# Kernel optimization log

Measured on AMD Instinct MI355X. Metric: run time of the kernel, lower is better.

The kernel has to match this reference:

```python
import jax, jax.numpy as jnp
import numpy as np

B, S, E, H, D = 2, 4096, 512, 8, 64  # batch, seq, embed, heads, key_dim


def setup_inputs() -> dict:
    key = jax.random.key(0)
    ks = jax.random.split(key, 8)
    queries = jax.random.normal(ks[0], (B, S, E), dtype=jnp.float32)
    keys = jax.random.normal(ks[1], (B, S, E), dtype=jnp.float32)
    values = jax.random.normal(ks[2], (B, S, E), dtype=jnp.float32)
    mask = jax.random.randint(ks[3], (B, H, S, S), 0, 2).astype(bool)
    scale = 1.0 / np.sqrt(E)
    Wq = jax.random.normal(ks[4], (E, H * D), dtype=jnp.float32) * scale
    Wk = jax.random.normal(ks[5], (E, H * D), dtype=jnp.float32) * scale
    Wv = jax.random.normal(ks[6], (E, H * D), dtype=jnp.float32) * scale
    Wo = jax.random.normal(ks[7], (H * D, E), dtype=jnp.float32) * scale
    return {"queries": queries, "keys": keys, "values": values, "mask": mask,
            "Wq": Wq, "Wk": Wk, "Wv": Wv, "Wo": Wo}


def reference(queries, keys, values, mask, Wq, Wk, Wv, Wo):
    # QKV projections (no bias), reshape to heads: (B, S, H, D)
    q = (queries @ Wq).reshape(B, -1, H, D)
    k = (keys @ Wk).reshape(B, -1, H, D)
    v = (values @ Wv).reshape(B, -1, H, D)
    # scores: (B, H, Sq, Sk)
    scores = jnp.einsum("bqhd,bkhd->bhqk", q, k) / jnp.sqrt(jnp.float32(D))
    scores = jnp.where(mask, jnp.float32(-1e10), scores)
    attn = jax.nn.softmax(scores, axis=-1)
    out = jnp.einsum("bhqk,bkhd->bqhd", attn, v).reshape(B, -1, H * D)
    return out @ Wo
```

## Files before the change

### kernel.cpp

```cpp
#include <hip/hip_runtime.h>
#include <hip/hip_bf16.h>

#define NB 2
#define NS 4096
#define NE 512
#define NH 8
#define ND 64
#define NHD 512

typedef __attribute__((ext_vector_type(8))) short short8;
typedef __attribute__((ext_vector_type(4))) float floatx4;

#define MFMA16(a, b, c) __builtin_amdgcn_mfma_f32_16x16x32_bf16((a), (b), (c), 0, 0, 0)

union Cvt8 { uint4 u; short8 s; };
static __device__ __forceinline__ short8 ld8(const __hip_bfloat16* p) {
  Cvt8 c; c.u = *(const uint4*)p; return c.s;
}
union BH { __hip_bfloat16 h; short s; };
static __device__ __forceinline__ short f2bs(float x) {
  BH u; u.h = __float2bfloat16(x); return u.s;
}

__global__ __launch_bounds__(256) void mask_pack(const int* __restrict__ mask,
                                                 unsigned long long* __restrict__ bits) {
  const int lane = threadIdx.x & 63;
  const long wid = (long)((blockIdx.x * 256 + threadIdx.x) >> 6);
  const long base = wid * 512;
  const int* p = mask + base * 64 + lane;
  for (int i = 0; i < 512; i += 4) {
    const int m0 = p[(long)(i + 0) * 64];
    const int m1 = p[(long)(i + 1) * 64];
    const int m2 = p[(long)(i + 2) * 64];
    const int m3 = p[(long)(i + 3) * 64];
    const unsigned long long b0 = __ballot(m0 != 0);
    const unsigned long long b1 = __ballot(m1 != 0);
    const unsigned long long b2 = __ballot(m2 != 0);
    const unsigned long long b3 = __ballot(m3 != 0);
    if (lane == 0) {
      *(ulonglong2*)(bits + base + i) = ulonglong2{b0, b1};
      *(ulonglong2*)(bits + base + i + 2) = ulonglong2{b2, b3};
    }
  }
}

__global__ __launch_bounds__(256) void wconv(
    const float* w0, const float* w1, const float* w2, const float* w3,
    __hip_bfloat16* t0, __hip_bfloat16* t1,
    __hip_bfloat16* t2, __hip_bfloat16* t3) {
  __shared__ __hip_bfloat16 tile[64][72];
  const float* src;
  __hip_bfloat16* dst;
  switch (blockIdx.z) {
    case 0: src = w0; dst = t0; break;
    case 1: src = w1; dst = t1; break;
    case 2: src = w2; dst = t2; break;
    default: src = w3; dst = t3; break;
  }
  const int tx = threadIdx.x & 63, ty = threadIdx.x >> 6;
  const int n0 = blockIdx.x * 64, k0 = blockIdx.y * 64;
  for (int r = ty; r < 64; r += 4)
    tile[r][tx] = __float2bfloat16(src[(long)(k0 + r) * 512 + n0 + tx]);
  __syncthreads();
  for (int r = ty; r < 64; r += 4)
    dst[(long)(n0 + r) * 512 + k0 + tx] = tile[tx][r];
}

__global__ __launch_bounds__(256) void gemm_qkv(
    const float* A0, const float* A1, const float* A2,
    const __hip_bfloat16* W0, const __hip_bfloat16* W1, const __hip_bfloat16* W2,
    __hip_bfloat16* O0, __hip_bfloat16* O1, __hip_bfloat16* O2) {
  const float* A;
  const __hip_bfloat16* Wt;
  __hip_bfloat16* O;
  switch (blockIdx.z) {
    case 0: A = A0; Wt = W0; O = O0; break;
    case 1: A = A1; Wt = W1; O = O1; break;
    default: A = A2; Wt = W2; O = O2; break;
  }
  const int lane = threadIdx.x & 63;
  const int w = threadIdx.x >> 6;
  const int c = lane & 15, g = lane >> 4;
  const int m0 = blockIdx.x * 64 + w * 16;
  const int n0 = blockIdx.y * 64;

  floatx4 acc[4] = {};
  const float* ap = A + (long)(m0 + c) * 512 + g * 8;
  const __hip_bfloat16* wp = Wt + (long)(n0 + c) * 512 + g * 8;
  for (int ks = 0; ks < 512; ks += 32) {
    const float4 f0 = *(const float4*)(ap + ks);
    const float4 f1 = *(const float4*)(ap + ks + 4);
    short8 a;
    a[0] = f2bs(f0.x); a[1] = f2bs(f0.y); a[2] = f2bs(f0.z); a[3] = f2bs(f0.w);
    a[4] = f2bs(f1.x); a[5] = f2bs(f1.y); a[6] = f2bs(f1.z); a[7] = f2bs(f1.w);
#pragma unroll
    for (int t = 0; t < 4; ++t) {
      short8 b = ld8(wp + t * 16 * 512 + ks);
      acc[t] = MFMA16(a, b, acc[t]);
    }
  }
  const float sc = (blockIdx.z == 0) ? 0.125f : 1.0f;
#pragma unroll
  for (int t = 0; t < 4; ++t) {
#pragma unroll
    for (int r = 0; r < 4; ++r) {
      const int m = m0 + g * 4 + r;
      const int n = n0 + t * 16 + c;
      const int bb = m >> 12, s = m & 4095, h = n >> 6, d = n & 63;
      O[(((long)bb * NH + h) * NS + s) * ND + d] = __float2bfloat16(acc[t][r] * sc);
    }
  }
}

#define VPAD 72
__device__ __forceinline__ int vswz(int row) { return ((row >> 3) & 7) * 8; }

__global__ __launch_bounds__(256) void flash_attn(
    const __hip_bfloat16* Q, const __hip_bfloat16* K, const __hip_bfloat16* V,
    const unsigned long long* __restrict__ Mb, __hip_bfloat16* AO) {
  __shared__ __hip_bfloat16 Ks[64 * VPAD];
  __shared__ __hip_bfloat16 Vt[64 * VPAD];
  __shared__ __hip_bfloat16 Pb[4 * 16 * VPAD];

  const int tid = threadIdx.x;
  const int lane = tid & 63, w = tid >> 6;
  const int c = lane & 15, g = lane >> 4;
  const int bz = blockIdx.z, hy = blockIdx.y;
  const int q0 = blockIdx.x * 64 + w * 16;
  const long headbase = ((long)bz * NH + hy) * NS;
  const unsigned long long* mrp0 = Mb + ((headbase + q0 + g * 4) << 6);

  const short8 qf0 = ld8(Q + (headbase + q0 + c) * ND + g * 8);
  const short8 qf1 = ld8(Q + (headbase + q0 + c) * ND + 32 + g * 8);

  floatx4 oacc[4] = {};
  float m_i[4], l_i[4];
#pragma unroll
  for (int r = 0; r < 4; ++r) { m_i[r] = -1e30f; l_i[r] = 0.f; }
  __hip_bfloat16* Pw = Pb + w * 16 * VPAD;

  for (int kt = 0; kt < 64; ++kt) {
    const int k0 = kt * 64;
#pragma unroll
    for (int it = 0; it < 2; ++it) {
      const int chunk = tid + it * 256;
      const int kc = chunk >> 3;
      const int dd = (chunk & 7) * 8;
      const long gbase = (headbase + k0 + kc) * ND + dd;
      *(uint4*)&Ks[kc * VPAD + dd] = *(const uint4*)(K + gbase);
      uint4 vv = *(const uint4*)(V + gbase);
      const __hip_bfloat16* ve = (const __hip_bfloat16*)&vv;
#pragma unroll
      for (int j = 0; j < 8; ++j) {
        const int row = dd + j;
        Vt[row * VPAD + (kc ^ vswz(row))] = ve[j];
      }
    }
    __syncthreads();

    unsigned long long mrow[4];
    mrow[0] = mrp0[kt];
    mrow[1] = mrp0[64 + kt];
    mrow[2] = mrp0[128 + kt];
    mrow[3] = mrp0[192 + kt];

    floatx4 sacc[4] = {};
#pragma unroll
    for (int t = 0; t < 4; ++t) {
      short8 b0 = ld8(&Ks[(t * 16 + c) * VPAD + g * 8]);
      sacc[t] = MFMA16(qf0, b0, sacc[t]);
      short8 b1 = ld8(&Ks[(t * 16 + c) * VPAD + 32 + g * 8]);
      sacc[t] = MFMA16(qf1, b1, sacc[t]);
    }

    float mx[4];
#pragma unroll
    for (int r = 0; r < 4; ++r) {
      const unsigned long long ms = mrow[r] >> c;
      float s0 = ((unsigned)ms & 1u) ? -1e10f : sacc[0][r];
      float s1 = ((unsigned)(ms >> 16) & 1u) ? -1e10f : sacc[1][r];
      float s2 = ((unsigned)(ms >> 32) & 1u) ? -1e10f : sacc[2][r];
      float s3 = ((unsigned)(ms >> 48) & 1u) ? -1e10f : sacc[3][r];
      sacc[0][r] = s0; sacc[1][r] = s1; sacc[2][r] = s2; sacc[3][r] = s3;
      float mxr = fmaxf(fmaxf(s0, s1), fmaxf(s2, s3));
#pragma unroll
      for (int off = 1; off < 16; off <<= 1)
        mxr = fmaxf(mxr, __shfl_xor(mxr, off));
      mx[r] = mxr;
    }

    const bool grow = (mx[0] > m_i[0]) | (mx[1] > m_i[1]) |
                      (mx[2] > m_i[2]) | (mx[3] > m_i[3]);
    if (__ballot(grow) != 0ull) {
      float alpha[4];
#pragma unroll
      for (int r = 0; r < 4; ++r) {
        const float mn = fmaxf(m_i[r], mx[r]);
        const float al = __expf(m_i[r] - mn);
        float ps = 0.f;
#pragma unroll
        for (int t = 0; t < 4; ++t) {
          const float p = __expf(sacc[t][r] - mn);
          sacc[t][r] = p;
          ps += p;
        }
#pragma unroll
        for (int off = 1; off < 16; off <<= 1)
          ps += __shfl_xor(ps, off);
        m_i[r] = mn;
        l_i[r] = l_i[r] * al + ps;
        alpha[r] = al;
      }
#pragma unroll
      for (int t = 0; t < 4; ++t)
#pragma unroll
        for (int r = 0; r < 4; ++r) oacc[t][r] *= alpha[r];
    } else {
#pragma unroll
      for (int r = 0; r < 4; ++r) {
        float ps = 0.f;
#pragma unroll
        for (int t = 0; t < 4; ++t) {
          const float p = __expf(sacc[t][r] - m_i[r]);
          sacc[t][r] = p;
          ps += p;
        }
#pragma unroll
        for (int off = 1; off < 16; off <<= 1)
          ps += __shfl_xor(ps, off);
        l_i[r] += ps;
      }
    }

#pragma unroll
    for (int r = 0; r < 4; ++r)
#pragma unroll
      for (int t = 0; t < 4; ++t)
        Pw[(g * 4 + r) * VPAD + t * 16 + c] = __float2bfloat16(sacc[t][r]);

#pragma unroll
    for (int ks2 = 0; ks2 < 2; ++ks2) {
      short8 af = ld8(&Pw[c * VPAD + ks2 * 32 + g * 8]);
#pragma unroll
      for (int t = 0; t < 4; ++t) {
        const int row = t * 16 + c;
        short8 bf = ld8(&Vt[row * VPAD + ((ks2 * 32 + g * 8) ^ vswz(row))]);
        oacc[t] = MFMA16(af, bf, oacc[t]);
      }
    }
    __syncthreads();
  }

#pragma unroll
  for (int t = 0; t < 4; ++t) {
#pragma unroll
    for (int r = 0; r < 4; ++r) {
      const int qrow = q0 + g * 4 + r;
      const float v = oacc[t][r] / l_i[r];
      AO[((long)bz * NS + qrow) * NHD + hy * 64 + t * 16 + c] = __float2bfloat16(v);
    }
  }
}

__global__ __launch_bounds__(256) void gemm_out(
    const __hip_bfloat16* A, const __hip_bfloat16* Wt, float* O) {
  const int lane = threadIdx.x & 63;
  const int w = threadIdx.x >> 6;
  const int c = lane & 15, g = lane >> 4;
  const int m0 = blockIdx.x * 64 + w * 16;
  const int n0 = blockIdx.y * 64;

  floatx4 acc[4] = {};
  const __hip_bfloat16* ap = A + (long)(m0 + c) * 512 + g * 8;
  const __hip_bfloat16* wp = Wt + (long)(n0 + c) * 512 + g * 8;
  for (int ks = 0; ks < 512; ks += 32) {
    short8 a = ld8(ap + ks);
#pragma unroll
    for (int t = 0; t < 4; ++t) {
      short8 b = ld8(wp + t * 16 * 512 + ks);
      acc[t] = MFMA16(a, b, acc[t]);
    }
  }
#pragma unroll
  for (int t = 0; t < 4; ++t)
#pragma unroll
    for (int r = 0; r < 4; ++r)
      O[(long)(m0 + g * 4 + r) * 512 + n0 + t * 16 + c] = acc[t][r];
}

extern "C" void kernel_launch(void* const* d_in, const int* in_sizes, int n_in,
                              void* d_out, int out_size, void* d_ws, size_t ws_size,
                              hipStream_t stream) {
  const float* q_in = (const float*)d_in[0];
  const float* k_in = (const float*)d_in[1];
  const float* v_in = (const float*)d_in[2];
  const int* mask = (const int*)d_in[3];
  const float* Wq = (const float*)d_in[4];
  const float* Wk = (const float*)d_in[5];
  const float* Wv = (const float*)d_in[6];
  const float* Wo = (const float*)d_in[7];
  float* out = (float*)d_out;

  char* base = (char*)d_ws;
  const size_t MB = 1u << 20;
  __hip_bfloat16* wtq = (__hip_bfloat16*)(base);
  __hip_bfloat16* wtk = (__hip_bfloat16*)(base + 512 * 1024);
  __hip_bfloat16* wtv = (__hip_bfloat16*)(base + 1 * MB);
  __hip_bfloat16* wto = (__hip_bfloat16*)(base + 1 * MB + 512 * 1024);
  __hip_bfloat16* qp = (__hip_bfloat16*)(base + 2 * MB);
  __hip_bfloat16* kp = (__hip_bfloat16*)(base + 10 * MB);
  __hip_bfloat16* vp = (__hip_bfloat16*)(base + 18 * MB);
  __hip_bfloat16* ao = (__hip_bfloat16*)(base + 26 * MB);
  unsigned long long* mb = (unsigned long long*)(base + 34 * MB);

  mask_pack<<<dim3(2048), 256, 0, stream>>>(mask, mb);
  wconv<<<dim3(8, 8, 4), 256, 0, stream>>>(Wq, Wk, Wv, Wo, wtq, wtk, wtv, wto);
  gemm_qkv<<<dim3(128, 8, 3), 256, 0, stream>>>(
      q_in, k_in, v_in, wtq, wtk, wtv, qp, kp, vp);
  flash_attn<<<dim3(NS / 64, NH, NB), 256, 0, stream>>>(qp, kp, vp, mb, ao);
  gemm_out<<<dim3(128, 8), 256, 0, stream>>>(ao, wto, out);
}
```

Before: 1.897 ms.

## Rewrite flash attention with 32x32 MFMA, transposed scores and register-resident P

The attention kernel now uses 32x32x16 bf16 MFMA tiles, with each wave handling 32 query rows and each block handling 128 queries. Scores are computed transposed (K as the A operand), so each lane owns one query row. That makes the softmax reductions mostly lane-local, and a single mask word per lane replaces four. P is packed to bf16 in registers and swapped between lane halves with shuffles instead of going through shared memory. The online-softmax rescale is skipped unless the max grows by more than 8, which trades some numerical headroom for fewer rescale passes. The grid is halved, which reduces K/V reloads per query but also lowers the block count and occupancy.

```diff
diff --git a/kernel.cpp b/kernel.cpp
--- a/kernel.cpp
+++ b/kernel.cpp
@@ -10,8 +10,10 @@
 
 typedef __attribute__((ext_vector_type(8))) short short8;
 typedef __attribute__((ext_vector_type(4))) float floatx4;
+typedef __attribute__((ext_vector_type(16))) float f32x16;
 
 #define MFMA16(a, b, c) __builtin_amdgcn_mfma_f32_16x16x32_bf16((a), (b), (c), 0, 0, 0)
+#define MFMA32(a, b, c) __builtin_amdgcn_mfma_f32_32x32x16_bf16((a), (b), (c), 0, 0, 0)
 
 union Cvt8 { uint4 u; short8 s; };
 static __device__ __forceinline__ short8 ld8(const __hip_bfloat16* p) {
@@ -20,6 +22,11 @@
 union BH { __hip_bfloat16 h; short s; };
 static __device__ __forceinline__ short f2bs(float x) {
   BH u; u.h = __float2bfloat16(x); return u.s;
+}
+static __device__ __forceinline__ unsigned pk2(float a, float b) {
+  unsigned d;
+  asm("v_cvt_pk_bf16_f32 %0, %1, %2" : "=v"(d) : "v"(a), "v"(b));
+  return d;
 }
 
 __global__ __launch_bounds__(256) void mask_pack(const int* __restrict__ mask,
@@ -120,24 +127,22 @@
     const unsigned long long* __restrict__ Mb, __hip_bfloat16* AO) {
   __shared__ __hip_bfloat16 Ks[64 * VPAD];
   __shared__ __hip_bfloat16 Vt[64 * VPAD];
-  __shared__ __hip_bfloat16 Pb[4 * 16 * VPAD];
 
   const int tid = threadIdx.x;
   const int lane = tid & 63, w = tid >> 6;
-  const int c = lane & 15, g = lane >> 4;
+  const int ql = lane & 31, hl = lane >> 5;
   const int bz = blockIdx.z, hy = blockIdx.y;
-  const int q0 = blockIdx.x * 64 + w * 16;
+  const int q0 = blockIdx.x * 128 + w * 32;
   const long headbase = ((long)bz * NH + hy) * NS;
-  const unsigned long long* mrp0 = Mb + ((headbase + q0 + g * 4) << 6);
-
-  const short8 qf0 = ld8(Q + (headbase + q0 + c) * ND + g * 8);
-  const short8 qf1 = ld8(Q + (headbase + q0 + c) * ND + 32 + g * 8);
-
-  floatx4 oacc[4] = {};
-  float m_i[4], l_i[4];
-#pragma unroll
-  for (int r = 0; r < 4; ++r) { m_i[r] = -1e30f; l_i[r] = 0.f; }
-  __hip_bfloat16* Pw = Pb + w * 16 * VPAD;
+
+  short8 qf[4];
+#pragma unroll
+  for (int ds = 0; ds < 4; ++ds)
+    qf[ds] = ld8(Q + (headbase + q0 + ql) * ND + ds * 16 + hl * 8);
+
+  f32x16 oacc0 = {}, oacc1 = {};
+  float m_i = -1e30f, l_i = 0.f;
+  const unsigned long long* mrp = Mb + ((headbase + q0 + ql) << 6);
 
   for (int kt = 0; kt < 64; ++kt) {
     const int k0 = kt * 64;
@@ -156,109 +161,93 @@
         Vt[row * VPAD + (kc ^ vswz(row))] = ve[j];
       }
     }
+    const unsigned long long mword = mrp[kt];
     __syncthreads();
 
-    unsigned long long mrow[4];
-    mrow[0] = mrp0[kt];
-    mrow[1] = mrp0[64 + kt];
-    mrow[2] = mrp0[128 + kt];
-    mrow[3] = mrp0[192 + kt];
-
-    floatx4 sacc[4] = {};
-#pragma unroll
-    for (int t = 0; t < 4; ++t) {
-      short8 b0 = ld8(&Ks[(t * 16 + c) * VPAD + g * 8]);
-      sacc[t] = MFMA16(qf0, b0, sacc[t]);
-      short8 b1 = ld8(&Ks[(t * 16 + c) * VPAD + 32 + g * 8]);
-      sacc[t] = MFMA16(qf1, b1, sacc[t]);
-    }
-
-    float mx[4];
-#pragma unroll
-    for (int r = 0; r < 4; ++r) {
-      const unsigned long long ms = mrow[r] >> c;
-      float s0 = ((unsigned)ms & 1u) ? -1e10f : sacc[0][r];
-      float s1 = ((unsigned)(ms >> 16) & 1u) ? -1e10f : sacc[1][r];
-      float s2 = ((unsigned)(ms >> 32) & 1u) ? -1e10f : sacc[2][r];
-      float s3 = ((unsigned)(ms >> 48) & 1u) ? -1e10f : sacc[3][r];
-      sacc[0][r] = s0; sacc[1][r] = s1; sacc[2][r] = s2; sacc[3][r] = s3;
-      float mxr = fmaxf(fmaxf(s0, s1), fmaxf(s2, s3));
-#pragma unroll
-      for (int off = 1; off < 16; off <<= 1)
-        mxr = fmaxf(mxr, __shfl_xor(mxr, off));
-      mx[r] = mxr;
-    }
-
-    const bool grow = (mx[0] > m_i[0]) | (mx[1] > m_i[1]) |
-                      (mx[2] > m_i[2]) | (mx[3] > m_i[3]);
-    if (__ballot(grow) != 0ull) {
-      float alpha[4];
-#pragma unroll
-      for (int r = 0; r < 4; ++r) {
-        const float mn = fmaxf(m_i[r], mx[r]);
-        const float al = __expf(m_i[r] - mn);
-        float ps = 0.f;
-#pragma unroll
-        for (int t = 0; t < 4; ++t) {
-          const float p = __expf(sacc[t][r] - mn);
-          sacc[t][r] = p;
-          ps += p;
-        }
-#pragma unroll
-        for (int off = 1; off < 16; off <<= 1)
-          ps += __shfl_xor(ps, off);
-        m_i[r] = mn;
-        l_i[r] = l_i[r] * al + ps;
-        alpha[r] = al;
+    f32x16 s0 = {}, s1 = {};
+#pragma unroll
+    for (int ds = 0; ds < 4; ++ds) {
+      short8 a0 = ld8(&Ks[ql * VPAD + ds * 16 + hl * 8]);
+      s0 = MFMA32(a0, qf[ds], s0);
+      short8 a1 = ld8(&Ks[(32 + ql) * VPAD + ds * 16 + hl * 8]);
+      s1 = MFMA32(a1, qf[ds], s1);
+    }
+
+    const unsigned long long wsh = mword >> (hl * 4);
+    const unsigned mlo = (unsigned)wsh;
+    const unsigned mhi = (unsigned)(wsh >> 32);
+    float mt = -1e30f;
+#pragma unroll
+    for (int r = 0; r < 16; ++r) {
+      const int idx = (r & 3) + 8 * (r >> 2);
+      const float a0 = ((mlo >> idx) & 1u) ? -1e10f : s0[r];
+      const float a1 = ((mhi >> idx) & 1u) ? -1e10f : s1[r];
+      s0[r] = a0; s1[r] = a1;
+      mt = fmaxf(mt, fmaxf(a0, a1));
+    }
+    mt = fmaxf(mt, __shfl_xor(mt, 32));
+
+    if (__ballot(mt > m_i + 8.0f) != 0ull) {
+      const float mn = fmaxf(m_i, mt);
+      const float al = __expf(m_i - mn);
+      m_i = mn;
+      l_i *= al;
+#pragma unroll
+      for (int r = 0; r < 16; ++r) {
+        const float ab = __shfl(al, (r & 3) + 8 * (r >> 2) + 4 * hl);
+        oacc0[r] *= ab;
+        oacc1[r] *= ab;
       }
-#pragma unroll
-      for (int t = 0; t < 4; ++t)
-#pragma unroll
-        for (int r = 0; r < 4; ++r) oacc[t][r] *= alpha[r];
-    } else {
-#pragma unroll
-      for (int r = 0; r < 4; ++r) {
-        float ps = 0.f;
-#pragma unroll
-        for (int t = 0; t < 4; ++t) {
-          const float p = __expf(sacc[t][r] - m_i[r]);
-          sacc[t][r] = p;
-          ps += p;
-        }
-#pragma unroll
-        for (int off = 1; off < 16; off <<= 1)
-          ps += __shfl_xor(ps, off);
-        l_i[r] += ps;
-      }
-    }
-
-#pragma unroll
-    for (int r = 0; r < 4; ++r)
-#pragma unroll
-      for (int t = 0; t < 4; ++t)
-        Pw[(g * 4 + r) * VPAD + t * 16 + c] = __float2bfloat16(sacc[t][r]);
-
-#pragma unroll
-    for (int ks2 = 0; ks2 < 2; ++ks2) {
-      short8 af = ld8(&Pw[c * VPAD + ks2 * 32 + g * 8]);
-#pragma unroll
-      for (int t = 0; t < 4; ++t) {
-        const int row = t * 16 + c;
-        short8 bf = ld8(&Vt[row * VPAD + ((ks2 * 32 + g * 8) ^ vswz(row))]);
-        oacc[t] = MFMA16(af, bf, oacc[t]);
-      }
+    }
+
+    float ss = 0.f;
+#pragma unroll
+    for (int r = 0; r < 16; ++r) {
+      const float p0 = __expf(s0[r] - m_i);
+      const float p1 = __expf(s1[r] - m_i);
+      s0[r] = p0; s1[r] = p1;
+      ss += p0 + p1;
+    }
+    ss += __shfl_xor(ss, 32);
+    l_i += ss;
+
+#pragma unroll
+    for (int ks = 0; ks < 4; ++ks) {
+      float pp[8];
+#pragma unroll
+      for (int j = 0; j < 8; ++j)
+        pp[j] = (ks < 2) ? ((ks & 1) ? s0[8 + j] : s0[j])
+                         : ((ks & 1) ? s1[8 + j] : s1[j]);
+      const unsigned pk01 = pk2(pp[0], pp[1]);
+      const unsigned pk23 = pk2(pp[2], pp[3]);
+      const unsigned pk45 = pk2(pp[4], pp[5]);
+      const unsigned pk67 = pk2(pp[6], pp[7]);
+      const unsigned send1 = hl ? pk01 : pk45;
+      const unsigned send2 = hl ? pk23 : pk67;
+      const unsigned recv1 = __shfl_xor(send1, 32);
+      const unsigned recv2 = __shfl_xor(send2, 32);
+      Cvt8 pc;
+      pc.u = make_uint4(hl ? recv1 : pk01,
+                        hl ? recv2 : pk23,
+                        hl ? pk45 : recv1,
+                        hl ? pk67 : recv2);
+      const int cb = ks * 16 + hl * 8;
+      const short8 v0 = ld8(&Vt[ql * VPAD + (cb ^ vswz(ql))]);
+      oacc0 = MFMA32(pc.s, v0, oacc0);
+      const short8 v1 = ld8(&Vt[(32 + ql) * VPAD + (cb ^ vswz(32 + ql))]);
+      oacc1 = MFMA32(pc.s, v1, oacc1);
     }
     __syncthreads();
   }
 
 #pragma unroll
-  for (int t = 0; t < 4; ++t) {
-#pragma unroll
-    for (int r = 0; r < 4; ++r) {
-      const int qrow = q0 + g * 4 + r;
-      const float v = oacc[t][r] / l_i[r];
-      AO[((long)bz * NS + qrow) * NHD + hy * 64 + t * 16 + c] = __float2bfloat16(v);
-    }
+  for (int r = 0; r < 16; ++r) {
+    const int cr = (r & 3) + 8 * (r >> 2) + 4 * hl;
+    const float lb = __shfl(l_i, cr);
+    const float inv = 1.0f / lb;
+    const long obase = ((long)bz * NS + q0 + cr) * NHD + hy * 64;
+    AO[obase + ql] = __float2bfloat16(oacc0[r] * inv);
+    AO[obase + 32 + ql] = __float2bfloat16(oacc1[r] * inv);
   }
 }
 
@@ -317,6 +306,6 @@
   wconv<<<dim3(8, 8, 4), 256, 0, stream>>>(Wq, Wk, Wv, Wo, wtq, wtk, wtv, wto);
   gemm_qkv<<<dim3(128, 8, 3), 256, 0, stream>>>(
       q_in, k_in, v_in, wtq, wtk, wtv, qp, kp, vp);
-  flash_attn<<<dim3(NS / 64, NH, NB), 256, 0, stream>>>(qp, kp, vp, mb, ao);
+  flash_attn<<<dim3(NS / 128, NH, NB), 256, 0, stream>>>(qp, kp, vp, mb, ao);
   gemm_out<<<dim3(128, 8), 256, 0, stream>>>(ao, wto, out);
 }
```

Result: faster. 1.752 ms (-7.6%).
